# Optimization experiments

Hardware: AMD Instinct MI355X
Metric: run time of the kernel (lower is better)

## Reference

```python
import jax, jax.numpy as jnp
import numpy as np

L, H, NH, B, S = 6, 768, 12, 4, 1024
D = H // NH
SCALE = 1.0 / np.sqrt(D)
EPS = 1e-5


def setup_inputs() -> dict:
    key = jax.random.key(0)
    ks = jax.random.split(key, 20)
    std = np.sqrt(2.0 / (5.0 * H)).astype(np.float32)
    w = lambda k, shape: (jax.random.normal(k, shape, jnp.float32) * std)
    x = jax.random.normal(ks[0], (B, S, H), jnp.float32)
    lengths = jnp.array([1024, 896, 768, 640])  # no fully-masked rows
    pad_mask = jnp.arange(S)[None, :] >= lengths[:, None]  # True = padding
    inp = {
        "x": x,
        "pad_mask": pad_mask,
        "Wq": w(ks[1], (L, H, H)), "bq": jnp.zeros((L, H), jnp.float32),
        "Wk": w(ks[2], (L, H, H)), "bk": w(ks[3], (L, H)) * 0.1,
        "Wv": w(ks[4], (L, H, H)), "bv": w(ks[5], (L, H)) * 0.1,
        "Wo": w(ks[6], (L, H, H)), "bo": jnp.zeros((L, H), jnp.float32),
        "ln1_g": jnp.ones((L, H), jnp.float32), "ln1_b": jnp.zeros((L, H), jnp.float32),
        "ln2_g": jnp.ones((L, H), jnp.float32), "ln2_b": jnp.zeros((L, H), jnp.float32),
        "W1": w(ks[7], (L, 8 * H, H)), "b1": jnp.zeros((L, 8 * H), jnp.float32),
        "W2": w(ks[8], (L, H, 4 * H)), "b2": jnp.zeros((L, H), jnp.float32),
        "out_g": jnp.ones((H,), jnp.float32), "out_b": jnp.zeros((H,), jnp.float32),
    }
    return inp


def _ln(x, g, b):
    m = jnp.mean(x, axis=-1, keepdims=True)
    v = jnp.mean(jnp.square(x - m), axis=-1, keepdims=True)
    return (x - m) * jax.lax.rsqrt(v + EPS) * g + b


def _encoder(x, pad_mask, params):
    def layer(x, p):
        (Wq, bq, Wk, bk, Wv, bv, Wo, bo, g1, be1, g2, be2, W1, b1, W2, b2) = p
        Bz, Sl, Hd = x.shape
        xn = _ln(x, g1, be1)
        q = (xn @ Wq.T + bq).reshape(Bz, Sl, NH, D)
        k = (xn @ Wk.T + bk).reshape(Bz, Sl, NH, D)
        v = (xn @ Wv.T + bv).reshape(Bz, Sl, NH, D)
        scores = jnp.einsum('bqhd,bkhd->bhqk', q, k) * SCALE
        scores = jnp.where(pad_mask[:, None, None, :], -jnp.inf, scores)
        probs = jax.nn.softmax(scores, axis=-1)
        av = jnp.einsum('bhqk,bkhd->bqhd', probs, v).reshape(Bz, Sl, Hd)
        x = x + (av @ Wo.T + bo)
        xn = _ln(x, g2, be2)
        h = xn @ W1.T + b1
        u, gate = jnp.split(h, 2, axis=-1)
        x = x + (u * jax.nn.gelu(gate, approximate=False)) @ W2.T + b2
        return x, None

    x, _ = jax.lax.scan(layer, x, params)
    return x


def reference(x, pad_mask, Wq, bq, Wk, bk, Wv, bv, Wo, bo,
              ln1_g, ln1_b, ln2_g, ln2_b, W1, b1, W2, b2, out_g, out_b):
    params = (Wq, bq, Wk, bk, Wv, bv, Wo, bo,
              ln1_g, ln1_b, ln2_g, ln2_b, W1, b1, W2, b2)
    x = _encoder(x, pad_mask, params)
    return _ln(x, out_g, out_b)
```

## Files before the change

kernel.cpp:

```cpp
#include <hip/hip_runtime.h>

typedef unsigned short u16;
typedef __bf16 bf16x8 __attribute__((ext_vector_type(8)));
typedef unsigned short us8 __attribute__((ext_vector_type(8)));
typedef unsigned short us4 __attribute__((ext_vector_type(4)));
typedef float f32x4 __attribute__((ext_vector_type(4)));

typedef __attribute__((address_space(3))) unsigned int as3_uint;
typedef const __attribute__((address_space(1))) unsigned int as1_cuint;

__device__ __forceinline__ u16 f2bf(float f) {
    unsigned u = __float_as_uint(f);
    u += 0x7FFFu + ((u >> 16) & 1u);
    return (u16)(u >> 16);
}
__device__ __forceinline__ float bf2f(u16 h) {
    return __uint_as_float(((unsigned)h) << 16);
}
__device__ __forceinline__ bf16x8 ld8(const u16* p) {
    return __builtin_bit_cast(bf16x8, *(const us8*)p);
}
#define MFMA16(a, b, c) __builtin_amdgcn_mfma_f32_16x16x32_bf16(a, b, c, 0, 0, 0)

__device__ __forceinline__ void glds16(const void* g, void* l) {
    __builtin_amdgcn_global_load_lds((as1_cuint*)g, (as3_uint*)l, 16, 0, 0);
}

__global__ void detect_k(const unsigned* __restrict__ pm, int* __restrict__ len4) {
    __shared__ int isbool;
    const int t = threadIdx.x;
    if (t == 0) isbool = 0;
    __syncthreads();
    unsigned orv = pm[t] | pm[256 + t] | pm[512 + t] | pm[768 + t];
    if (orv & 0xFFFFFF00u) atomicOr(&isbool, 1);
    __syncthreads();
    const int w = t >> 6, l = t & 63;
    int cnt = 0;
    if (isbool) {
        const unsigned char* p8 = (const unsigned char*)pm;
        for (int i = l; i < 1024; i += 64) cnt += (p8[w * 1024 + i] == 0) ? 1 : 0;
    } else {
        for (int i = l; i < 1024; i += 64) cnt += (pm[w * 1024 + i] == 0u) ? 1 : 0;
    }
#pragma unroll
    for (int m = 1; m < 64; m <<= 1) cnt += __shfl_xor(cnt, m);
    if (l == 0) {
        int c = cnt;
        if (c < 1) c = 1;
        if (c > 1024) c = 1024;
        len4[w] = c;
    }
}

__global__ __launch_bounds__(256) void conv_k(
    const float* __restrict__ Wq, const float* __restrict__ Wk,
    const float* __restrict__ Wv, const float* __restrict__ Wo,
    const float* __restrict__ W1, const float* __restrict__ W2,
    const float* __restrict__ bq, const float* __restrict__ bk,
    const float* __restrict__ bv,
    u16* __restrict__ wall, float* __restrict__ bqkv6) {
    const int lyr = blockIdx.y;
    const int idx = blockIdx.x * 256 + threadIdx.x;
    const size_t e = (size_t)idx * 4;
    const float* src;
    if (e < 2359296u) {
        int which = (int)(e / 589824u);
        size_t off = e % 589824u;
        const float* m = (which == 0) ? Wq : (which == 1) ? Wk : (which == 2) ? Wv : Wo;
        src = m + (size_t)lyr * 589824u + off;
    } else if (e < 7077888u) {
        src = W1 + (size_t)lyr * 4718592u + (e - 2359296u);
    } else {
        src = W2 + (size_t)lyr * 2359296u + (e - 7077888u);
    }
    u16* dst = wall + (size_t)lyr * 9437184u + e;
    float4 v = *(const float4*)src;
    us4 o;
    o[0] = f2bf(v.x); o[1] = f2bf(v.y); o[2] = f2bf(v.z); o[3] = f2bf(v.w);
    *(us4*)dst = o;
    if (idx < 2304) {
        float bb = (idx < 768) ? bq[lyr * 768 + idx]
                 : (idx < 1536) ? bk[lyr * 768 + idx - 768]
                                : bv[lyr * 768 + idx - 1536];
        bqkv6[lyr * 2304 + idx] = bb;
    }
}

template <int OUTF>
__global__ __launch_bounds__(256) void ln_k(const float* __restrict__ x,
                                            const float* __restrict__ gm,
                                            const float* __restrict__ bt,
                                            void* __restrict__ outp) {
    const int w = threadIdx.x >> 6, l = threadIdx.x & 63;
    const int row = blockIdx.x * 4 + w;
    const float4* xr = (const float4*)(x + (size_t)row * 768);
    float4 v[3];
    float s = 0.f, ss = 0.f;
#pragma unroll
    for (int i = 0; i < 3; ++i) {
        v[i] = xr[i * 64 + l];
        s += v[i].x + v[i].y + v[i].z + v[i].w;
        ss += v[i].x * v[i].x + v[i].y * v[i].y + v[i].z * v[i].z + v[i].w * v[i].w;
    }
#pragma unroll
    for (int m = 1; m < 64; m <<= 1) {
        s += __shfl_xor(s, m);
        ss += __shfl_xor(ss, m);
    }
    const float mean = s * (1.f / 768.f);
    float var = ss * (1.f / 768.f) - mean * mean;
    var = fmaxf(var, 0.f);
    const float rs = rsqrtf(var + 1e-5f);
    const float4* g4 = (const float4*)gm;
    const float4* b4 = (const float4*)bt;
#pragma unroll
    for (int i = 0; i < 3; ++i) {
        float4 gg = g4[i * 64 + l], bb = b4[i * 64 + l];
        float o0 = (v[i].x - mean) * rs * gg.x + bb.x;
        float o1 = (v[i].y - mean) * rs * gg.y + bb.y;
        float o2 = (v[i].z - mean) * rs * gg.z + bb.z;
        float o3 = (v[i].w - mean) * rs * gg.w + bb.w;
        if (OUTF) {
            ((float4*)outp)[(size_t)row * 192 + i * 64 + l] = make_float4(o0, o1, o2, o3);
        } else {
            us4 pk;
            pk[0] = f2bf(o0); pk[1] = f2bf(o1); pk[2] = f2bf(o2); pk[3] = f2bf(o3);
            ((us4*)outp)[(size_t)row * 192 + i * 64 + l] = pk;
        }
    }
}

template <int VAR, int NF, int CHAIN, int PRO>
__device__ __forceinline__ void g256_body(
    const u16* __restrict__ Ab, const u16* __restrict__ Bb0,
    const u16* __restrict__ Bb1,
    const u16* __restrict__ AbN, const u16* __restrict__ Bb0N,
    const u16* __restrict__ Bb1N,
    const float* __restrict__ bias, u16* __restrict__ outp,
    u16* __restrict__ vT, int ldout, int ncol0, int m0,
    u16 (&lds)[2][4][8192]) {
    const int tid = threadIdx.x;
    const int w = tid >> 6, l = tid & 63, ax = l & 15, gx = l >> 4;
    const int wr = w >> 2, wc = w & 3;
    const int K = 768;

    const int row0 = tid >> 2, cc0 = (tid & 3) ^ ((row0 >> 1) & 3);
    const int row1 = 128 + row0, cc1 = (tid & 3) ^ ((row1 >> 1) & 3);
    const size_t goA0 = (size_t)row0 * K + cc0 * 8;
    const size_t goA1 = (size_t)row1 * K + cc1 * 8;

    auto stage = [&](int u, int kt, int nxt) {
        const int kh = u & 1;
        const size_t koff = (size_t)kt * 64 + kh * 32;
        u16* d = (u16*)&lds[kt & 1][u][0];
        const u16* A_ = nxt ? AbN : Ab;
        const u16* B0_ = nxt ? Bb0N : Bb0;
        const u16* B1_ = nxt ? Bb1N : Bb1;
        if (u < 2) {
            glds16(A_ + goA0 + koff, d + tid * 8);
            glds16(A_ + goA1 + koff, d + (512 + tid) * 8);
        } else {
            glds16(B0_ + goA0 + koff, d + tid * 8);
            glds16(B1_ + goA1 + koff, d + (512 + tid) * 8);
        }
    };

    bf16x8 rav[4], rbv[NF];
    f32x4 acc[8][NF] = {};

    auto phase = [&](int buf, int q, int kh, int readB, int vm, int su, int skt,
                     int nxt) {
        if (vm == 8) asm volatile("s_waitcnt vmcnt(8)" ::: "memory");
        else if (vm == 4) asm volatile("s_waitcnt vmcnt(4)" ::: "memory");
        else if (vm == 0) asm volatile("s_waitcnt vmcnt(0)" ::: "memory");
        __builtin_amdgcn_s_barrier();
        if (readB) {
#pragma unroll
            for (int j = 0; j < NF; ++j) {
                int row;
                if (VAR == 0) row = wc * (16 * NF) + j * 16 + ax;
                else row = ((j >= NF / 2) ? 128 : 0) + wc * (8 * NF) +
                           (j % (NF / 2)) * 16 + ax;
                rbv[j] = ld8(&lds[buf][2 + kh][row * 32 + ((gx ^ ((row >> 1) & 3)) * 8)]);
            }
        }
#pragma unroll
        for (int mf = 0; mf < 4; ++mf) {
            int row = wr * 128 + q * 64 + mf * 16 + ax;
            rav[mf] = ld8(&lds[buf][kh][row * 32 + ((gx ^ ((row >> 1) & 3)) * 8)]);
        }
        if (su >= 0) stage(su, skt, nxt);
        asm volatile("s_waitcnt lgkmcnt(0)" ::: "memory");
        __builtin_amdgcn_sched_barrier(0);
        __builtin_amdgcn_s_setprio(1);
#pragma unroll
        for (int mf = 0; mf < 4; ++mf)
#pragma unroll
            for (int j = 0; j < NF; ++j)
                acc[q * 4 + mf][j] = MFMA16(rav[mf], rbv[j], acc[q * 4 + mf][j]);
        __builtin_amdgcn_s_setprio(0);
    };

    if (PRO) {
        stage(0, 0, 0); stage(2, 0, 0); stage(1, 0, 0);
        stage(3, 0, 0); stage(0, 1, 0); stage(2, 1, 0);
    }

#pragma unroll 1
    for (int t = 0; t < 5; ++t) {
        const int O = 2 * t + 1, E2 = 2 * t + 2, O2 = 2 * t + 3;
        phase(0, 0, 0, 1, 8, 1, O, 0);
        phase(0, 1, 0, 0, -1, 3, O, 0);
        phase(0, 0, 1, 1, 8, 0, E2, 0);
        phase(0, 1, 1, 0, -1, 2, E2, 0);
        phase(1, 0, 0, 1, 8, 1, E2, 0);
        phase(1, 1, 0, 0, -1, 3, E2, 0);
        phase(1, 0, 1, 1, 8, 0, O2, 0);
        phase(1, 1, 1, 0, -1, 2, O2, 0);
    }
    if (CHAIN) {
        phase(0, 0, 0, 1, 8, 1, 11, 0);
        phase(0, 1, 0, 0, -1, 3, 11, 0);
        phase(0, 0, 1, 1, 8, 0, 0, 1);
        phase(0, 1, 1, 0, -1, 2, 0, 1);
        phase(1, 0, 0, 1, 8, 1, 0, 1);
        phase(1, 1, 0, 0, -1, 3, 0, 1);
        phase(1, 0, 1, 1, 8, 0, 1, 1);
        phase(1, 1, 1, 0, -1, 2, 1, 1);
    } else {
        phase(0, 0, 0, 1, 8, 1, 11, 0);
        phase(0, 1, 0, 0, -1, 3, 11, 0);
        phase(0, 0, 1, 1, 8, -1, 0, 0);
        phase(0, 1, 1, 0, -1, -1, 0, 0);
        phase(1, 0, 0, 1, 4, -1, 0, 0);
        phase(1, 1, 0, 0, -1, -1, 0, 0);
        phase(1, 0, 1, 1, 0, -1, 0, 0);
        phase(1, 1, 1, 0, -1, -1, 0, 0);
    }

    const int rowb = m0 + wr * 128;
    if (VAR == 0) {
        if (ncol0 >= 1536) {
#pragma unroll
            for (int j = 0; j < NF; ++j) {
                const int col = ncol0 + wc * (16 * NF) + j * 16 + ax;
                const float bn = bias[col];
                u16* vcol = vT + (size_t)(col - 1536) * 4096;
#pragma unroll
                for (int am = 0; am < 8; ++am) {
                    const int rb_ = rowb + am * 16 + 4 * gx;
                    us4 pk;
#pragma unroll
                    for (int r = 0; r < 4; ++r) pk[r] = f2bf(acc[am][j][r] + bn);
                    *(us4*)(vcol + rb_) = pk;
                }
            }
        } else {
#pragma unroll
            for (int j = 0; j < NF; ++j) {
                const int col = ncol0 + wc * (16 * NF) + j * 16 + ax;
                const float bn = bias[col];
#pragma unroll
                for (int am = 0; am < 8; ++am) {
                    const int rb_ = rowb + am * 16 + 4 * gx;
#pragma unroll
                    for (int r = 0; r < 4; ++r)
                        outp[(size_t)(rb_ + r) * ldout + col] = f2bf(acc[am][j][r] + bn);
                }
            }
        }
    } else {
        const int P = NF / 2;
#pragma unroll
        for (int nf = 0; nf < NF / 2; ++nf) {
            const int col = ncol0 + wc * (16 * P) + nf * 16 + ax;
            const float bu_ = bias[col], bg_ = bias[3072 + col];
#pragma unroll
            for (int am = 0; am < 8; ++am) {
                const int rb_ = rowb + am * 16 + 4 * gx;
#pragma unroll
                for (int r = 0; r < 4; ++r) {
                    float uu = acc[am][nf][r] + bu_;
                    float gg = acc[am][P + nf][r] + bg_;
                    float gel = 0.5f * gg * (1.f + erff(gg * 0.70710678118f));
                    outp[(size_t)(rb_ + r) * ldout + col] = f2bf(uu * gel);
                }
            }
        }
    }
}

__global__ __launch_bounds__(512, 2) void qkv256_k(
    const u16* __restrict__ A, const u16* __restrict__ W,
    const float* __restrict__ bias, u16* __restrict__ outp,
    u16* __restrict__ vT) {
    __shared__ __align__(16) u16 lds[2][4][8192];
    const int bid = blockIdx.x;
    const int swz = (bid & 7) * 24 + (bid >> 3);
    const int nb = swz >> 4, mb = swz & 15;
    const int m0 = mb * 256;
    const u16* Ab = A + (size_t)m0 * 768;
    const u16* Bb0 = W + (size_t)(nb * 192) * 768;
    g256_body<0, 3, 0, 1>(Ab, Bb0, Bb0, nullptr, nullptr, nullptr,
                          bias, outp, vT, 2304, nb * 192, m0, lds);
}

__global__ __launch_bounds__(512, 2) void ffn1_k(
    const u16* __restrict__ A, const u16* __restrict__ W,
    const float* __restrict__ bias, u16* __restrict__ outp) {
    __shared__ __align__(16) u16 lds[2][4][8192];
    const int bid = blockIdx.x;
    const int swz = (bid & 7) * 32 + (bid >> 3);
    const int nb = swz >> 4, mb = swz & 15;
    const int m0 = mb * 256;
    const u16* Ab = A + (size_t)m0 * 768;
    const u16* Bb0 = W + (size_t)(nb * 128) * 768;
    const u16* Bb1 = W + (size_t)(3072 + nb * 128 - 128) * 768;
    const u16* Bb0h = W + (size_t)(2048 + nb * 64) * 768;
    const u16* Bb1h = W + (size_t)(5120 + nb * 64 - 128) * 768;
    g256_body<1, 4, 1, 1>(Ab, Bb0, Bb1, Ab, Bb0h, Bb1h,
                          bias, outp, nullptr, 3072, nb * 128, m0, lds);
    g256_body<1, 2, 0, 0>(Ab, Bb0h, Bb1h, nullptr, nullptr, nullptr,
                          bias, outp, nullptr, 3072, 2048 + nb * 64, m0, lds);
}

template <int EPI>
__global__ __launch_bounds__(512) void gemm_k(
    const u16* __restrict__ A, const u16* __restrict__ W,
    const float* __restrict__ bias, const float* __restrict__ resid,
    void* __restrict__ outp, int N, int K) {
    __shared__ __align__(16) u16 smem[2 * 8192 + 2 * 6144];
    const int tid = threadIdx.x;
    const int w = tid >> 6, l = tid & 63, a = l & 15, g = l >> 4;
    const int wr = w >> 2, wc = (w >> 1) & 1, kz = w & 1;
    const int m0 = blockIdx.y * 128, n0 = blockIdx.x * 96;
    f32x4 acc[4][3] = {};
    const int nk = K >> 6;

    auto stage = [&](int kt, int buf) {
        const int k0 = kt * 64;
        u16* dA = smem + buf * 8192;
        u16* dB = smem + 16384 + buf * 6144;
#pragma unroll
        for (int i = 0; i < 2; ++i) {
            int c = i * 512 + tid;
            int row = c >> 3, cc = c & 7, c8 = cc ^ (row & 7);
            glds16(A + (size_t)(m0 + row) * K + k0 + c8 * 8, dA + c * 8);
        }
        {
            int c = tid;
            int row = c >> 3, cc = c & 7, c8 = cc ^ (row & 7);
            glds16(W + (size_t)(n0 + row) * K + k0 + c8 * 8, dB + c * 8);
        }
        {
            int c = 512 + (tid & 255);
            int row = c >> 3, cc = c & 7, c8 = cc ^ (row & 7);
            glds16(W + (size_t)(n0 + row) * K + k0 + c8 * 8, dB + c * 8);
        }
    };

    stage(0, 0);
    int cur = 0;
    for (int kt = 0; kt < nk; ++kt) {
        if (kt + 1 < nk) {
            stage(kt + 1, cur ^ 1);
            __builtin_amdgcn_sched_barrier(0);
            asm volatile("s_waitcnt vmcnt(4)" ::: "memory");
        } else {
            __builtin_amdgcn_sched_barrier(0);
            asm volatile("s_waitcnt vmcnt(0)" ::: "memory");
        }
        __builtin_amdgcn_s_barrier();
        const u16* dA = smem + cur * 8192;
        const u16* dB = smem + 16384 + cur * 6144;
        bf16x8 af[4], bv_[3];
#pragma unroll
        for (int m = 0; m < 4; ++m) {
            int row = wr * 64 + m * 16 + a;
            af[m] = ld8(&dA[row * 64 + (((kz * 4 + g) ^ (a & 7)) * 8)]);
        }
#pragma unroll
        for (int n = 0; n < 3; ++n) {
            int row = wc * 48 + n * 16 + a;
            bv_[n] = ld8(&dB[row * 64 + (((kz * 4 + g) ^ (a & 7)) * 8)]);
        }
        asm volatile("s_waitcnt lgkmcnt(0)" ::: "memory");
        __builtin_amdgcn_sched_barrier(0);
        __builtin_amdgcn_s_setprio(1);
#pragma unroll
        for (int m = 0; m < 4; ++m)
#pragma unroll
            for (int n = 0; n < 3; ++n)
                acc[m][n] = MFMA16(af[m], bv_[n], acc[m][n]);
        __builtin_amdgcn_s_setprio(0);
        __builtin_amdgcn_s_barrier();
        cur ^= 1;
    }

    __syncthreads();
    float* sc = (float*)smem;
    const int quad = wr * 2 + wc;
    if (kz == 1) {
#pragma unroll
        for (int m = 0; m < 4; ++m)
#pragma unroll
            for (int n = 0; n < 3; ++n)
#pragma unroll
                for (int r = 0; r < 4; ++r)
                    sc[quad * 3136 + (m * 16 + 4 * g + r) * 49 + n * 16 + a] =
                        acc[m][n][r];
    }
    __syncthreads();
    if (kz == 0) {
        u16* outu = (u16*)outp;
        float* outf = (float*)outp;
        const int row0 = m0 + wr * 64, col0 = n0 + wc * 48;
#pragma unroll
        for (int n = 0; n < 3; ++n) {
            const int col = col0 + n * 16 + a;
            const float bn = bias[col];
#pragma unroll
            for (int m = 0; m < 4; ++m) {
                const int rb = row0 + m * 16 + 4 * g;
#pragma unroll
                for (int r = 0; r < 4; ++r) {
                    const size_t off = (size_t)(rb + r) * N + col;
                    float vv = acc[m][n][r] + bn +
                               sc[quad * 3136 + (m * 16 + 4 * g + r) * 49 + n * 16 + a];
                    if constexpr (EPI == 0) {
                        outu[off] = f2bf(vv);
                    } else {
                        outf[off] = vv + resid[off];
                    }
                }
            }
        }
    }
}

__global__ __launch_bounds__(256) void attn_k(const u16* __restrict__ qkv,
                                              const u16* __restrict__ vT,
                                              u16* __restrict__ av,
                                              const int* __restrict__ len4) {
    __shared__ __align__(16) u16 Ks[2][64 * 64];
    __shared__ __align__(16) u16 Vt[2][64 * 64];
    __shared__ __align__(16) u16 Ps[4][16 * 64];
    const int tid = threadIdx.x;
    const int w = tid >> 6, l = tid & 63, a = l & 15, g = l >> 4;
    const int qb = blockIdx.x, h = blockIdx.y, b = blockIdx.z;
    const size_t rowQ = (size_t)(b * 1024 + qb * 64 + w * 16 + a);
    const u16* qp = qkv + rowQ * 2304 + h * 64;
    bf16x8 qf[2];
    qf[0] = __builtin_bit_cast(bf16x8, *(const us8*)(qp + g * 8));
    qf[1] = __builtin_bit_cast(bf16x8, *(const us8*)(qp + 32 + g * 8));
    f32x4 O[4] = {};
    float m_r[4], l_r[4];
#pragma unroll
    for (int r = 0; r < 4; ++r) { m_r[r] = -1e30f; l_r[r] = 0.f; }
    const int length = len4[b];
    const int nkt = (length + 63) >> 6;

    auto stageK = [&](int kt, int buf) {
#pragma unroll
        for (int i = 0; i < 2; ++i) {
            int c = i * 256 + tid;
            int row = c >> 3, cc = c & 7, c8 = cc ^ (row & 7);
            glds16(qkv + (size_t)(b * 1024 + kt * 64 + row) * 2304 + 768 + h * 64 + c8 * 8,
                   &Ks[buf][c * 8]);
        }
    };
    us8 vv[2];
    auto loadV = [&](int kt) {
        const u16* vrow = vT + (size_t)(h * 64 + l) * 4096 + b * 1024 + kt * 64;
#pragma unroll
        for (int i = 0; i < 2; ++i) vv[i] = *(const us8*)(vrow + (w + 4 * i) * 8);
    };
    auto writeV = [&](int buf) {
#pragma unroll
        for (int i = 0; i < 2; ++i) {
            int kkc = w + 4 * i;
            int cc = kkc ^ (l & 7);
            *(us8*)&Vt[buf][l * 64 + cc * 8] = vv[i];
        }
    };

    stageK(0, 0);
    loadV(0);
    asm volatile("s_waitcnt vmcnt(0)" ::: "memory");
    writeV(0);
    __syncthreads();
    int buf = 0;
    for (int kt = 0; kt < nkt; ++kt) {
        const bool pf = (kt + 1 < nkt);
        if (pf) { stageK(kt + 1, buf ^ 1); loadV(kt + 1); }
        f32x4 s[4] = {};
#pragma unroll
        for (int ks = 0; ks < 2; ++ks) {
#pragma unroll
            for (int f = 0; f < 4; ++f) {
                int row = f * 16 + a;
                bf16x8 kf = ld8(&Ks[buf][row * 64 + (((ks * 4 + g) ^ (a & 7)) * 8)]);
                s[f] = MFMA16(qf[ks], kf, s[f]);
            }
        }
        float mloc[4] = {-1e30f, -1e30f, -1e30f, -1e30f};
#pragma unroll
        for (int f = 0; f < 4; ++f) {
            int kkg = kt * 64 + f * 16 + a;
            bool valid = kkg < length;
#pragma unroll
            for (int r = 0; r < 4; ++r) {
                float v = valid ? s[f][r] * 0.125f : -1e30f;
                s[f][r] = v;
                mloc[r] = fmaxf(mloc[r], v);
            }
        }
#pragma unroll
        for (int r = 0; r < 4; ++r) {
#pragma unroll
            for (int m = 1; m < 16; m <<= 1)
                mloc[r] = fmaxf(mloc[r], __shfl_xor(mloc[r], m));
        }
        float al[4], ps[4];
#pragma unroll
        for (int r = 0; r < 4; ++r) {
            float nm = fmaxf(m_r[r], mloc[r]);
            al[r] = __expf(m_r[r] - nm);
            m_r[r] = nm;
            ps[r] = 0.f;
        }
#pragma unroll
        for (int f = 0; f < 4; ++f)
#pragma unroll
            for (int r = 0; r < 4; ++r) {
                float p = __expf(s[f][r] - m_r[r]);
                s[f][r] = p;
                ps[r] += p;
            }
#pragma unroll
        for (int r = 0; r < 4; ++r) {
#pragma unroll
            for (int m = 1; m < 16; m <<= 1) ps[r] += __shfl_xor(ps[r], m);
            l_r[r] = l_r[r] * al[r] + ps[r];
        }
#pragma unroll
        for (int df = 0; df < 4; ++df)
#pragma unroll
            for (int r = 0; r < 4; ++r) O[df][r] *= al[r];
        if (pf) {
            asm volatile("s_waitcnt vmcnt(0)" ::: "memory");
            writeV(buf ^ 1);
        }
#pragma unroll
        for (int f = 0; f < 4; ++f)
#pragma unroll
            for (int r = 0; r < 4; ++r) {
                int prow = 4 * g + r;
                int cc = (2 * f + (a >> 3)) ^ (prow & 7);
                Ps[w][prow * 64 + cc * 8 + (a & 7)] = f2bf(s[f][r]);
            }
        asm volatile("s_waitcnt lgkmcnt(0)" ::: "memory");
        __builtin_amdgcn_sched_barrier(0);
#pragma unroll
        for (int ks = 0; ks < 2; ++ks) {
            bf16x8 pf_ = ld8(&Ps[w][a * 64 + (((ks * 4 + g) ^ (a & 7)) * 8)]);
#pragma unroll
            for (int df = 0; df < 4; ++df) {
                int vrow = df * 16 + a;
                bf16x8 vf = ld8(&Vt[buf][vrow * 64 + (((ks * 4 + g) ^ (a & 7)) * 8)]);
                O[df] = MFMA16(pf_, vf, O[df]);
            }
        }
        __syncthreads();
        buf ^= 1;
    }
#pragma unroll
    for (int df = 0; df < 4; ++df) {
        int col = h * 64 + df * 16 + a;
#pragma unroll
        for (int r = 0; r < 4; ++r) {
            int row = b * 1024 + qb * 64 + w * 16 + 4 * g + r;
            av[(size_t)row * 768 + col] = f2bf(O[df][r] / l_r[r]);
        }
    }
}

extern "C" void kernel_launch(void* const* d_in, const int* in_sizes, int n_in,
                              void* d_out, int out_size, void* d_ws, size_t ws_size,
                              hipStream_t stream) {
    const float* x_in = (const float*)d_in[0];
    const unsigned* pm = (const unsigned*)d_in[1];
    const float* Wq = (const float*)d_in[2];
    const float* bq = (const float*)d_in[3];
    const float* Wk = (const float*)d_in[4];
    const float* bk = (const float*)d_in[5];
    const float* Wv = (const float*)d_in[6];
    const float* bv = (const float*)d_in[7];
    const float* Wo = (const float*)d_in[8];
    const float* bo = (const float*)d_in[9];
    const float* g1 = (const float*)d_in[10];
    const float* be1 = (const float*)d_in[11];
    const float* g2 = (const float*)d_in[12];
    const float* be2 = (const float*)d_in[13];
    const float* W1 = (const float*)d_in[14];
    const float* b1 = (const float*)d_in[15];
    const float* W2 = (const float*)d_in[16];
    const float* b2 = (const float*)d_in[17];
    const float* og = (const float*)d_in[18];
    const float* ob = (const float*)d_in[19];

    char* ws = (char*)d_ws;
    u16* wall  = (u16*)(ws + 0);
    float* bqkv6 = (float*)(ws + 113246208);
    int* len4  = (int*)(ws + 113301504);
    float* xbuf = (float*)(ws + 113301760);
    u16* xn    = (u16*)(ws + 125884672);
    u16* qkv   = (u16*)(ws + 132176128);
    u16* avb   = (u16*)(ws + 151050496);
    u16* ub    = (u16*)(ws + 157341952);
    u16* vT    = (u16*)(ws + 157341952);

    detect_k<<<1, 256, 0, stream>>>(pm, len4);
    conv_k<<<dim3(9216, 6), 256, 0, stream>>>(Wq, Wk, Wv, Wo, W1, W2, bq, bk, bv,
                                              wall, bqkv6);
    for (int l = 0; l < 6; ++l) {
        u16* wl = wall + (size_t)l * 9437184u;
        const float* xcur = (l == 0) ? x_in : xbuf;
        ln_k<0><<<1024, 256, 0, stream>>>(xcur, g1 + l * 768, be1 + l * 768, xn);
        qkv256_k<<<192, 512, 0, stream>>>(xn, wl, bqkv6 + l * 2304, qkv, vT);
        attn_k<<<dim3(16, 12, 4), 256, 0, stream>>>(qkv, vT, avb, len4);
        gemm_k<1><<<dim3(8, 32), 512, 0, stream>>>(avb, wl + 3 * 589824, bo + l * 768,
                                                   xcur, xbuf, 768, 768);
        ln_k<0><<<1024, 256, 0, stream>>>(xbuf, g2 + l * 768, be2 + l * 768, xn);
        ffn1_k<<<256, 512, 0, stream>>>(xn, wl + 2359296, b1 + l * 6144, ub);
        gemm_k<1><<<dim3(8, 32), 512, 0, stream>>>(ub, wl + 7077888, b2 + l * 768, xbuf,
                                                   xbuf, 768, 3072);
    }
    ln_k<1><<<1024, 256, 0, stream>>>(xbuf, og, ob, d_out);
}
```

Measured before the change: 1.180 ms.

## Overlap per-layer weight conversion with the FFN2 GEMM via extra grid blocks

The upfront fp32-to-bf16 conversion now covers only layer 0. Each later layer's weights are converted by extra blocks (z>0) added to the previous layer's FFN2 gemm launch, so the conversion traffic can run alongside the compute-bound GEMM on idle CUs. The gemm kernel gains branch logic and extra parameters. Conversion blocks may compete with GEMM blocks for bandwidth and CUs, and they could be scheduled ahead of them.

```diff
diff --git a/kernel.cpp b/kernel.cpp
--- a/kernel.cpp
+++ b/kernel.cpp
@@ -52,14 +52,13 @@
     }
 }
 
-__global__ __launch_bounds__(256) void conv_k(
+__global__ __launch_bounds__(256) void conv0_k(
     const float* __restrict__ Wq, const float* __restrict__ Wk,
     const float* __restrict__ Wv, const float* __restrict__ Wo,
     const float* __restrict__ W1, const float* __restrict__ W2,
     const float* __restrict__ bq, const float* __restrict__ bk,
     const float* __restrict__ bv,
     u16* __restrict__ wall, float* __restrict__ bqkv6) {
-    const int lyr = blockIdx.y;
     const int idx = blockIdx.x * 256 + threadIdx.x;
     const size_t e = (size_t)idx * 4;
     const float* src;
@@ -67,22 +66,25 @@
         int which = (int)(e / 589824u);
         size_t off = e % 589824u;
         const float* m = (which == 0) ? Wq : (which == 1) ? Wk : (which == 2) ? Wv : Wo;
-        src = m + (size_t)lyr * 589824u + off;
+        src = m + off;
     } else if (e < 7077888u) {
-        src = W1 + (size_t)lyr * 4718592u + (e - 2359296u);
+        src = W1 + (e - 2359296u);
     } else {
-        src = W2 + (size_t)lyr * 2359296u + (e - 7077888u);
-    }
-    u16* dst = wall + (size_t)lyr * 9437184u + e;
+        src = W2 + (e - 7077888u);
+    }
+    u16* dst = wall + e;
     float4 v = *(const float4*)src;
     us4 o;
     o[0] = f2bf(v.x); o[1] = f2bf(v.y); o[2] = f2bf(v.z); o[3] = f2bf(v.w);
     *(us4*)dst = o;
     if (idx < 2304) {
-        float bb = (idx < 768) ? bq[lyr * 768 + idx]
-                 : (idx < 1536) ? bk[lyr * 768 + idx - 768]
-                                : bv[lyr * 768 + idx - 1536];
-        bqkv6[lyr * 2304 + idx] = bb;
+#pragma unroll
+        for (int lyr = 0; lyr < 6; ++lyr) {
+            float bb = (idx < 768) ? bq[lyr * 768 + idx]
+                     : (idx < 1536) ? bk[lyr * 768 + idx - 768]
+                                    : bv[lyr * 768 + idx - 1536];
+            bqkv6[lyr * 2304 + idx] = bb;
+        }
     }
 }
 
@@ -328,8 +330,35 @@
 __global__ __launch_bounds__(512) void gemm_k(
     const u16* __restrict__ A, const u16* __restrict__ W,
     const float* __restrict__ bias, const float* __restrict__ resid,
-    void* __restrict__ outp, int N, int K) {
+    void* __restrict__ outp, int N, int K,
+    const float* __restrict__ cWq, const float* __restrict__ cWk,
+    const float* __restrict__ cWv, const float* __restrict__ cWo,
+    const float* __restrict__ cW1, const float* __restrict__ cW2,
+    u16* __restrict__ cwall, int cvtlyr) {
     __shared__ __align__(16) u16 smem[2 * 8192 + 2 * 6144];
+    if (blockIdx.z > 0) {
+        const int cid = ((int)blockIdx.z - 1) * 256 + (int)blockIdx.y * 8 +
+                        (int)blockIdx.x;
+        const size_t e = ((size_t)cid * 512 + threadIdx.x) * 4;
+        const float* src;
+        if (e < 2359296u) {
+            int which = (int)(e / 589824u);
+            size_t off = e % 589824u;
+            const float* m = (which == 0) ? cWq : (which == 1) ? cWk
+                           : (which == 2) ? cWv : cWo;
+            src = m + (size_t)cvtlyr * 589824u + off;
+        } else if (e < 7077888u) {
+            src = cW1 + (size_t)cvtlyr * 4718592u + (e - 2359296u);
+        } else {
+            src = cW2 + (size_t)cvtlyr * 2359296u + (e - 7077888u);
+        }
+        u16* dst = cwall + (size_t)cvtlyr * 9437184u + e;
+        float4 v = *(const float4*)src;
+        us4 o;
+        o[0] = f2bf(v.x); o[1] = f2bf(v.y); o[2] = f2bf(v.z); o[3] = f2bf(v.w);
+        *(us4*)dst = o;
+        return;
+    }
     const int tid = threadIdx.x;
     const int w = tid >> 6, l = tid & 63, a = l & 15, g = l >> 4;
     const int wr = w >> 2, wc = (w >> 1) & 1, kz = w & 1;
@@ -621,20 +650,23 @@
     u16* vT    = (u16*)(ws + 157341952);
 
     detect_k<<<1, 256, 0, stream>>>(pm, len4);
-    conv_k<<<dim3(9216, 6), 256, 0, stream>>>(Wq, Wk, Wv, Wo, W1, W2, bq, bk, bv,
-                                              wall, bqkv6);
+    conv0_k<<<9216, 256, 0, stream>>>(Wq, Wk, Wv, Wo, W1, W2, bq, bk, bv,
+                                      wall, bqkv6);
     for (int l = 0; l < 6; ++l) {
         u16* wl = wall + (size_t)l * 9437184u;
         const float* xcur = (l == 0) ? x_in : xbuf;
         ln_k<0><<<1024, 256, 0, stream>>>(xcur, g1 + l * 768, be1 + l * 768, xn);
         qkv256_k<<<192, 512, 0, stream>>>(xn, wl, bqkv6 + l * 2304, qkv, vT);
         attn_k<<<dim3(16, 12, 4), 256, 0, stream>>>(qkv, vT, avb, len4);
-        gemm_k<1><<<dim3(8, 32), 512, 0, stream>>>(avb, wl + 3 * 589824, bo + l * 768,
-                                                   xcur, xbuf, 768, 768);
+        gemm_k<1><<<dim3(8, 32, 1), 512, 0, stream>>>(
+            avb, wl + 3 * 589824, bo + l * 768, xcur, xbuf, 768, 768,
+            nullptr, nullptr, nullptr, nullptr, nullptr, nullptr, nullptr, 0);
         ln_k<0><<<1024, 256, 0, stream>>>(xbuf, g2 + l * 768, be2 + l * 768, xn);
         ffn1_k<<<256, 512, 0, stream>>>(xn, wl + 2359296, b1 + l * 6144, ub);
-        gemm_k<1><<<dim3(8, 32), 512, 0, stream>>>(ub, wl + 7077888, b2 + l * 768, xbuf,
-                                                   xbuf, 768, 3072);
+        const int zconv = (l < 5) ? 19 : 1;
+        gemm_k<1><<<dim3(8, 32, zconv), 512, 0, stream>>>(
+            ub, wl + 7077888, b2 + l * 768, xbuf, xbuf, 768, 3072,
+            Wq, Wk, Wv, Wo, W1, W2, wall, l + 1);
     }
     ln_k<1><<<1024, 256, 0, stream>>>(xbuf, og, ob, d_out);
 }
```

Result: faster. 1.124 ms (-4.7%).
